# Performance work log

Hardware: AMD Instinct MI355X
Metric: run time of the kernel (lower is better)

## Reference

```python
import jax, jax.numpy as jnp
import numpy as np

B, S, E = 2, 2048, 1024
H = 16
D = E // H  # head_dim = 64


def setup_inputs() -> dict:
    key = jax.random.key(0)
    ks = jax.random.split(key, 11)
    s = 1.0 / np.sqrt(E)
    return {
        "x": jax.random.normal(ks[0], (B, S, E), dtype=jnp.float32),
        "Wq": jax.random.uniform(ks[1], (E, E), jnp.float32, -s, s),
        "bq": jnp.zeros((E,), jnp.float32),
        "Wk": jax.random.uniform(ks[2], (E, E), jnp.float32, -s, s),
        "bk": jnp.zeros((E,), jnp.float32),
        "Wv": jax.random.uniform(ks[3], (E, E), jnp.float32, -s, s),
        "bv": jnp.zeros((E,), jnp.float32),
        "Wo": jax.random.uniform(ks[4], (E, E), jnp.float32, -s, s),
        "bo": jnp.zeros((E,), jnp.float32),
        "J_attn": jax.random.normal(ks[5], (H, D, D), jnp.float32) * 0.02,
        "lambda_attn": jnp.float32(0.5),
    }


def reference(x, Wq, bq, Wk, bk, Wv, bv, Wo, bo, J_attn, lambda_attn):
    b, s, _ = x.shape
    scale = jnp.sqrt(jnp.float32(D))

    def split_heads(y):  # [b,s,E] -> [b,H,s,D]
        return y.reshape(b, s, H, D).transpose(0, 2, 1, 3)

    Q = split_heads(x @ Wq.T + bq)
    K = split_heads(x @ Wk.T + bk)
    V = split_heads(x @ Wv.T + bv)

    attn_scores = jnp.einsum('bhid,bhjd->bhij', Q, K) / scale

    Qn = jnp.tanh(Q)
    Kn = jnp.tanh(K)
    # fold J into Qn first (small [H,D,D] contraction), then one big matmul
    QJ = jnp.einsum('bhid,hde->bhie', Qn, J_attn)
    delta = jnp.einsum('bhie,bhje->bhij', QJ, Kn)

    attn_scores = attn_scores + lambda_attn * delta
    attn_probs = jax.nn.softmax(attn_scores, axis=-1)

    out = jnp.einsum('bhij,bhjd->bhid', attn_probs, V)
    out = out.transpose(0, 2, 1, 3).reshape(b, s, E)
    return out @ Wo.T + bo
```

## Files before the change

kernel.cpp:

```cpp
#include <hip/hip_runtime.h>
#include <math.h>

#define NH 16

typedef __bf16 bf16x8 __attribute__((ext_vector_type(8)));
typedef float f32x4 __attribute__((ext_vector_type(4)));

__device__ __forceinline__ unsigned short f2bf(float f) {
  unsigned u = __float_as_uint(f);
  u += 0x7fffu + ((u >> 16) & 1u);
  return (unsigned short)(u >> 16);
}
__device__ __forceinline__ float bf2f(unsigned short h) {
  return __uint_as_float(((unsigned)h) << 16);
}
__device__ __forceinline__ float fexp2(float x) {
  return __builtin_amdgcn_exp2f(x);
}
__device__ __forceinline__ float fast_tanh16(float x) {
  return 1.f - 2.f * __builtin_amdgcn_rcpf(fexp2(16.f * x) + 1.f);
}
__device__ __forceinline__ void gl_lds16(const void* g, void* l) {
  __builtin_amdgcn_global_load_lds((const __attribute__((address_space(1))) void*)g,
                                   (__attribute__((address_space(3))) void*)l, 16, 0, 0);
}
union Frag8 { bf16x8 v; unsigned short u[8]; };
union FragU { bf16x8 v; unsigned u[4]; };
union FragQ { bf16x8 v; unsigned long long q[2]; };

__global__ __launch_bounds__(256) void prep_all(const float* __restrict__ x,
                                                const float* __restrict__ Wq,
                                                const float* __restrict__ Wk,
                                                const float* __restrict__ Wv,
                                                const float* __restrict__ Wo,
                                                const float* __restrict__ J,
                                                const float* __restrict__ lam_p,
                                                unsigned short* __restrict__ xh,
                                                unsigned short* __restrict__ wcat3,
                                                unsigned short* __restrict__ wocat,
                                                unsigned short* __restrict__ Jt)
{
  __shared__ float T[64][65];
  const int bid = blockIdx.x, tid = threadIdx.x;
  if (bid >= 8192) {
    const int h = bid - 8192;
    const float lam = lam_p[0] * 1.44269504f;
#pragma unroll
    for (int c = 0; c < 4; ++c) {
      int i = tid + c*256;
      int d = i >> 4, e4 = i & 15;
      float4 v = *(const float4*)&J[(size_t)h*4096 + d*64 + e4*4];
      T[d][e4*4+0] = v.x; T[d][e4*4+1] = v.y; T[d][e4*4+2] = v.z; T[d][e4*4+3] = v.w;
    }
    __syncthreads();
    const int e = tid >> 2, d0 = (tid & 3) * 16;
#pragma unroll
    for (int j4 = 0; j4 < 4; ++j4) {
      ushort4 o;
      o.x = f2bf(lam * T[d0+j4*4+0][e]);
      o.y = f2bf(lam * T[d0+j4*4+1][e]);
      o.z = f2bf(lam * T[d0+j4*4+2][e]);
      o.w = f2bf(lam * T[d0+j4*4+3][e]);
      *(ushort4*)&Jt[((size_t)h*64 + e)*64 + d0 + j4*4] = o;
    }
    return;
  }
  if (bid < 4096) {
    int i = bid * 256 + tid;
    float4 v = *(const float4*)&x[(size_t)i*4];
    ushort4 o;
    o.x = f2bf(v.x); o.y = f2bf(v.y); o.z = f2bf(v.z); o.w = f2bf(v.w);
    *(ushort4*)&xh[(size_t)i*4] = o;
  } else if (bid < 7168) {
    int i = (bid - 4096) * 256 + tid;
    int sel = i >> 18, loc = i & 262143;
    const float* src = (sel == 0) ? Wq : (sel == 1) ? Wk : Wv;
    float4 v = *(const float4*)&src[(size_t)loc*4];
    ushort4 o;
    o.x = f2bf(v.x); o.y = f2bf(v.y); o.z = f2bf(v.z); o.w = f2bf(v.w);
    *(ushort4*)&wcat3[(size_t)i*4] = o;
  } else {
    int i = (bid - 7168) * 256 + tid;
    int r = i >> 8, c = i & 255;
    float4 v = *(const float4*)&Wo[(size_t)r*1024 + c*4];
    ushort4 hi, lo;
    hi.x = f2bf(v.x); lo.x = f2bf(v.x - bf2f(hi.x));
    hi.y = f2bf(v.y); lo.y = f2bf(v.y - bf2f(hi.y));
    hi.z = f2bf(v.z); lo.z = f2bf(v.z - bf2f(hi.z));
    hi.w = f2bf(v.w); lo.w = f2bf(v.w - bf2f(hi.w));
    *(ushort4*)&wocat[(size_t)r*2048 + c*4]        = hi;
    *(ushort4*)&wocat[(size_t)r*2048 + 1024 + c*4] = lo;
  }
}

__global__ __launch_bounds__(256) void gemm_qkv(const unsigned short* __restrict__ A,
                                                const unsigned short* __restrict__ W,
                                                const float* __restrict__ bq,
                                                const float* __restrict__ bk,
                                                const float* __restrict__ bv,
                                                const unsigned short* __restrict__ Jt,
                                                unsigned short* __restrict__ Qcat,
                                                unsigned short* __restrict__ Kcat,
                                                unsigned short* __restrict__ Vt)
{
  __shared__ unsigned short S[32768];
  const int tid = threadIdx.x, lane = tid & 63, wq = tid >> 6;
  const int l15 = lane & 15, lq = lane >> 4;
  const int n0 = blockIdx.x * 128, m0 = blockIdx.y * 128;
  const int wr = (wq & 1) * 64, wc = (wq >> 1) * 64;
  const int mode = n0 >> 10;

  f32x4 acc[4][4];
#pragma unroll
  for (int mb = 0; mb < 4; ++mb)
#pragma unroll
    for (int nb = 0; nb < 4; ++nb) { f32x4 z = {0.f,0.f,0.f,0.f}; acc[mb][nb] = z; }

  const unsigned short* mat = (wq < 2) ? A : W;
  const int rbase = (wq < 2) ? m0 : n0;
  const int srow = lane >> 3, sslot = lane & 7;

  auto STAGE = [&](int buf, int k0) {
    unsigned short* lb = S + buf*16384 + (wq >> 1) * 8192;
#pragma unroll
    for (int t = 0; t < 8; ++t) {
      int row = (wq & 1) * 64 + t*8 + srow;
      int chunk = sslot ^ (row & 7);
      gl_lds16(mat + (size_t)(rbase + row)*1024 + k0 + chunk*8,
               lb + ((wq & 1) * 64 + t*8) * 64);
    }
  };

  int cur = 0;
  STAGE(0, 0);
  __syncthreads();

  for (int k0 = 0; k0 < 1024; k0 += 64) {
    if (k0 + 64 < 1024) STAGE(cur ^ 1, k0 + 64);
    const unsigned short* Sc = S + cur*16384;
#pragma unroll
    for (int kk = 0; kk < 2; ++kk) {
      int c = kk*4 + lq;
      bf16x8 af[4], bf_[4];
#pragma unroll
      for (int mb = 0; mb < 4; ++mb) {
        int m = wr + mb*16 + l15;
        af[mb] = *(const bf16x8*)&Sc[m*64 + (c ^ (m & 7))*8];
      }
#pragma unroll
      for (int nb = 0; nb < 4; ++nb) {
        int n = wc + nb*16 + l15;
        bf_[nb] = *(const bf16x8*)&Sc[8192 + n*64 + (c ^ (n & 7))*8];
      }
#pragma unroll
      for (int mb = 0; mb < 4; ++mb)
#pragma unroll
        for (int nb = 0; nb < 4; ++nb)
          acc[mb][nb] = __builtin_amdgcn_mfma_f32_16x16x32_bf16(af[mb], bf_[nb], acc[mb][nb], 0,0,0);
    }
    __syncthreads();
    cur ^= 1;
  }

  const float* bias = (mode == 0) ? bq : (mode == 1) ? bk : bv;
  float bvv[4];
#pragma unroll
  for (int nb = 0; nb < 4; ++nb) bvv[nb] = bias[((n0 & 1023) + wc + nb*16 + l15)];

  if (mode == 2) {
#pragma unroll
    for (int mb = 0; mb < 4; ++mb) {
      int mrow = m0 + wr + mb*16 + lq*4;
      int b = mrow >> 11, s0 = mrow & 2047;
#pragma unroll
      for (int nb = 0; nb < 4; ++nb) {
        int n = (n0 & 1023) + wc + nb*16 + l15;
        int h = n >> 6, d = n & 63;
        ushort4 o;
        o.x = f2bf(acc[mb][nb][0] + bvv[nb]);
        o.y = f2bf(acc[mb][nb][1] + bvv[nb]);
        o.z = f2bf(acc[mb][nb][2] + bvv[nb]);
        o.w = f2bf(acc[mb][nb][3] + bvv[nb]);
        *(ushort4*)&Vt[((size_t)(b*NH + h)*64 + d)*2048 + s0] = o;
      }
    }
    return;
  }

  if (mode == 1) {
#pragma unroll
    for (int mb = 0; mb < 4; ++mb) {
#pragma unroll
      for (int r = 0; r < 4; ++r) {
        int m = m0 + wr + mb*16 + lq*4 + r;
        int b = m >> 11, s = m & 2047;
#pragma unroll
        for (int nb = 0; nb < 4; ++nb) {
          float v = acc[mb][nb][r] + bvv[nb];
          int n = (n0 & 1023) + wc + nb*16 + l15;
          int h = n >> 6, d = n & 63;
          size_t row = ((size_t)(b*NH + h)*2048 + s)*128;
          Kcat[row + d]      = f2bf(v);
          Kcat[row + 64 + d] = f2bf(1.f - 2.f * __builtin_amdgcn_rcpf(__expf(2.f*v) + 1.f));
        }
      }
    }
    return;
  }

  unsigned short* T = S + wq * 4608;
#pragma unroll
  for (int mb = 0; mb < 4; ++mb) {
#pragma unroll
    for (int r = 0; r < 4; ++r) {
      int m = m0 + wr + mb*16 + lq*4 + r;
      int b = m >> 11, s = m & 2047;
#pragma unroll
      for (int nb = 0; nb < 4; ++nb) {
        float v = acc[mb][nb][r] + bvv[nb];
        int n = (n0 & 1023) + wc + nb*16 + l15;
        int h = n >> 6, d = n & 63;
        unsigned short qb = f2bf(v * 0.18033688f);
        Qcat[((size_t)(b*NH + h)*2048 + s)*128 + d] = qb;
        T[(mb*16 + lq*4 + r)*72 + d] = qb;
      }
    }
  }
  const int h = ((n0 & 1023) + wc) >> 6;
  bf16x8 jf2[4][2];
#pragma unroll
  for (int nb2 = 0; nb2 < 4; ++nb2)
#pragma unroll
    for (int kst = 0; kst < 2; ++kst)
      jf2[nb2][kst] = *(const bf16x8*)&Jt[((size_t)h*64 + nb2*16 + l15)*64 + kst*32 + lq*8];
#pragma unroll
  for (int mb = 0; mb < 4; ++mb) {
    Frag8 af2[2];
#pragma unroll
    for (int kst = 0; kst < 2; ++kst) {
      Frag8 raw;
      raw.v = *(const bf16x8*)&T[(mb*16 + l15)*72 + kst*32 + lq*8];
#pragma unroll
      for (int j = 0; j < 8; ++j) {
        float t = fast_tanh16(bf2f(raw.u[j]));
        af2[kst].u[j] = (unsigned short)(__float_as_uint(t) >> 16);
      }
    }
    f32x4 a2[4];
#pragma unroll
    for (int nb2 = 0; nb2 < 4; ++nb2) { f32x4 z = {0.f,0.f,0.f,0.f}; a2[nb2] = z; }
#pragma unroll
    for (int kst = 0; kst < 2; ++kst)
#pragma unroll
      for (int nb2 = 0; nb2 < 4; ++nb2)
        a2[nb2] = __builtin_amdgcn_mfma_f32_16x16x32_bf16(af2[kst].v, jf2[nb2][kst], a2[nb2], 0,0,0);
    int mrow = m0 + wr + mb*16 + lq*4;
    int b = mrow >> 11, s0 = mrow & 2047;
#pragma unroll
    for (int r = 0; r < 4; ++r) {
      size_t rowb = ((size_t)(b*NH + h)*2048 + s0 + r)*128 + 64;
#pragma unroll
      for (int nb2 = 0; nb2 < 4; ++nb2)
        Qcat[rowb + nb2*16 + l15] = f2bf(a2[nb2][r]);
    }
  }
}

__global__ __launch_bounds__(256, 4) void flash8(
    const unsigned short* __restrict__ Qcat, const unsigned short* __restrict__ Kcat,
    const unsigned short* __restrict__ Vt, unsigned short* __restrict__ attcat)
{
  __shared__ __align__(16) char smem[49152];
  unsigned short* Ks = (unsigned short*)smem;
  unsigned short* Vs = (unsigned short*)(smem + 32768);
  const int tid = threadIdx.x, lane = tid & 63, wq = tid >> 6;
  const int l15 = lane & 15, lq = lane >> 4;
  const int bid = blockIdx.x;
  const int bh = (((bid >> 3) & 3) << 3) | (bid & 7);
  const int inner = bid >> 5;
  const int row0 = inner * 128;

  Frag8 qf[2][4];
#pragma unroll
  for (int nb = 0; nb < 2; ++nb) {
    const unsigned short* qp = Qcat + ((size_t)(bh*2048 + row0 + wq*32 + nb*16 + l15))*128 + lq*8;
#pragma unroll
    for (int kst = 0; kst < 4; ++kst)
      qf[nb][kst].v = *(const bf16x8*)(qp + kst*32);
  }

  FragU ones;
  ones.u[0] = 0x3F803F80u; ones.u[1] = 0x3F803F80u;
  ones.u[2] = 0x3F803F80u; ones.u[3] = 0x3F803F80u;

  f32x4 o[4][2];
  f32x4 lacc[2];
  { f32x4 z = {0.f,0.f,0.f,0.f}; lacc[0] = z; lacc[1] = z; }
#pragma unroll
  for (int db = 0; db < 4; ++db)
#pragma unroll
    for (int nb = 0; nb < 2; ++nb) { f32x4 z = {0.f,0.f,0.f,0.f}; o[db][nb] = z; }

  const unsigned short* kgb = Kcat + ((size_t)bh*2048)*128;
  const unsigned short* vg  = Vt + (size_t)bh*64*2048;

  auto STAGE = [&](int buf, int jt) {
#pragma unroll
    for (int t = 0; t < 4; ++t) {
      int g = (wq*4 + t)*4 + (lane >> 4);
      int slot = lane & 15;
      int chunk = (slot & 8) | ((slot ^ g) & 7);
      gl_lds16(kgb + (size_t)(jt*64 + g)*128 + chunk*8, Ks + buf*8192 + (wq*4 + t)*512);
    }
#pragma unroll
    for (int t = 0; t < 2; ++t) {
      int rv = (wq*2 + t)*8 + (lane >> 3);
      int chunk = (lane & 7) ^ (rv & 7);
      gl_lds16(vg + (size_t)rv*2048 + jt*64 + chunk*8, Vs + buf*4096 + (wq*2 + t)*512);
    }
  };

  int cur = 0;
  STAGE(0, 0);
  __syncthreads();

  for (int jt = 0; jt < 32; ++jt) {
    if (jt + 1 < 32) STAGE(cur ^ 1, jt + 1);
    const unsigned short* ksb = Ks + cur*8192;
    const unsigned short* vsb = Vs + cur*4096;

#pragma unroll
    for (int t = 0; t < 2; ++t) {
      unsigned P2[2][2][2];
#pragma unroll
      for (int kk = 0; kk < 2; ++kk) {
        const int kb = 2*t + kk;
        bf16x8 af[4];
#pragma unroll
        for (int kst = 0; kst < 4; ++kst) {
          int key = kb*16 + l15;
          int c = kst*4 + lq;
          int slot = (c & 8) | ((c ^ key) & 7);
          af[kst] = *(const bf16x8*)&ksb[key*128 + slot*8];
        }
        f32x4 s[2];
        { f32x4 z = {0.f,0.f,0.f,0.f}; s[0] = z; s[1] = z; }
        __builtin_amdgcn_s_setprio(1);
#pragma unroll
        for (int kst = 0; kst < 4; ++kst) {
          s[0] = __builtin_amdgcn_mfma_f32_16x16x32_bf16(af[kst], qf[0][kst].v, s[0], 0,0,0);
          s[1] = __builtin_amdgcn_mfma_f32_16x16x32_bf16(af[kst], qf[1][kst].v, s[1], 0,0,0);
        }
        __builtin_amdgcn_s_setprio(0);
#pragma unroll
        for (int nb = 0; nb < 2; ++nb) {
          float e0 = fexp2(s[nb][0]), e1 = fexp2(s[nb][1]);
          float e2 = fexp2(s[nb][2]), e3 = fexp2(s[nb][3]);
          P2[nb][kk][0] = __builtin_amdgcn_perm(__float_as_uint(e1), __float_as_uint(e0), 0x07060302u);
          P2[nb][kk][1] = __builtin_amdgcn_perm(__float_as_uint(e3), __float_as_uint(e2), 0x07060302u);
        }
      }

      FragU bfr[2];
#pragma unroll
      for (int nb = 0; nb < 2; ++nb) {
        bfr[nb].u[0] = P2[nb][0][0];
        bfr[nb].u[1] = P2[nb][0][1];
        bfr[nb].u[2] = P2[nb][1][0];
        bfr[nb].u[3] = P2[nb][1][1];
      }
      __builtin_amdgcn_s_setprio(1);
      lacc[0] = __builtin_amdgcn_mfma_f32_16x16x32_bf16(ones.v, bfr[0].v, lacc[0], 0,0,0);
      lacc[1] = __builtin_amdgcn_mfma_f32_16x16x32_bf16(ones.v, bfr[1].v, lacc[1], 0,0,0);

      const int c0 = 4*t + (lq >> 1);
      const int woff = 4*(lq & 1);
#pragma unroll
      for (int db = 0; db < 4; ++db) {
        int d = db*16 + l15;
        FragQ va;
        va.q[0] = *(const unsigned long long*)&vsb[d*64 + ((c0     ^ (d & 7))*8) + woff];
        va.q[1] = *(const unsigned long long*)&vsb[d*64 + (((c0+2) ^ (d & 7))*8) + woff];
        o[db][0] = __builtin_amdgcn_mfma_f32_16x16x32_bf16(va.v, bfr[0].v, o[db][0], 0,0,0);
        o[db][1] = __builtin_amdgcn_mfma_f32_16x16x32_bf16(va.v, bfr[1].v, o[db][1], 0,0,0);
      }
      __builtin_amdgcn_s_setprio(0);
    }

    __syncthreads();
    cur ^= 1;
  }

  const int b = bh >> 4, h = bh & (NH-1);
  const float inv0 = 1.f / lacc[0][0];
  const float inv1 = 1.f / lacc[1][0];
  float* Ts = (float*)smem;
#pragma unroll
  for (int half = 0; half < 2; ++half) {
    __syncthreads();
    if ((wq >> 1) == half) {
#pragma unroll
      for (int nb = 0; nb < 2; ++nb) {
        const float inv = nb ? inv1 : inv0;
        const int rl = (wq & 1)*32 + nb*16 + l15;
#pragma unroll
        for (int db = 0; db < 4; ++db)
#pragma unroll
          for (int r = 0; r < 4; ++r)
            Ts[rl*65 + db*16 + lq*4 + r] = o[db][nb][r] * inv;
      }
    }
    __syncthreads();
    const int sl = tid >> 2, d0 = (tid & 3) * 16;
    const int srow = row0 + half*64 + sl;
    const size_t rb = ((size_t)(b*2048 + srow))*2048 + h*64;
#pragma unroll
    for (int j4 = 0; j4 < 4; ++j4) {
      float v0 = Ts[sl*65 + d0 + j4*4 + 0];
      float v1 = Ts[sl*65 + d0 + j4*4 + 1];
      float v2 = Ts[sl*65 + d0 + j4*4 + 2];
      float v3 = Ts[sl*65 + d0 + j4*4 + 3];
      ushort4 hi, lo;
      hi.x = f2bf(v0); lo.x = f2bf(v0 - bf2f(hi.x));
      hi.y = f2bf(v1); lo.y = f2bf(v1 - bf2f(hi.y));
      hi.z = f2bf(v2); lo.z = f2bf(v2 - bf2f(hi.z));
      hi.w = f2bf(v3); lo.w = f2bf(v3 - bf2f(hi.w));
      *(ushort4*)&attcat[rb + d0 + j4*4]        = hi;
      *(ushort4*)&attcat[rb + 1024 + d0 + j4*4] = lo;
    }
  }
}

__global__ __launch_bounds__(512) void gemm3b(const unsigned short* __restrict__ A,
                                              const unsigned short* __restrict__ W,
                                              const float* __restrict__ bias,
                                              float* __restrict__ out)
{
  __shared__ unsigned short S[65536];
  const int tid = threadIdx.x, lane = tid & 63, wid = tid >> 6;
  const int l15 = lane & 15, lq = lane >> 4;
  const int n0 = blockIdx.x * 128, m0 = blockIdx.y * 128;
  const int wrow = wid >> 2, wcol = wid & 3;

  f32x4 acc[4][2];
#pragma unroll
  for (int mb = 0; mb < 4; ++mb)
#pragma unroll
    for (int nb = 0; nb < 2; ++nb) { f32x4 z = {0.f,0.f,0.f,0.f}; acc[mb][nb] = z; }

  const int region = wid >> 1;
  const unsigned short* mat = (region < 2) ? A : W;
  const int rbase = (region < 2) ? m0 : n0;
  const int koff  = (region & 1) * 1024;
  const int rhalf = (wid & 1) * 64;
  const int srow = lane >> 3, sslot = lane & 7;

  auto STAGE = [&](int buf, int k0) {
    unsigned short* lb = S + buf*32768 + region*8192 + rhalf*64;
#pragma unroll
    for (int t = 0; t < 8; ++t) {
      int row = rhalf + t*8 + srow;
      int chunk = sslot ^ (row & 7);
      gl_lds16(mat + (size_t)(rbase + row)*2048 + koff + k0 + chunk*8,
               lb + t*512);
    }
  };

  int cur = 0;
  STAGE(0, 0);
  __syncthreads();

  for (int k0 = 0; k0 < 1024; k0 += 64) {
    if (k0 + 64 < 1024) STAGE(cur ^ 1, k0 + 64);
    const unsigned short* Sc = S + cur*32768;
#pragma unroll
    for (int kk = 0; kk < 2; ++kk) {
      int c = kk*4 + lq;
      bf16x8 ah[4], al[4], bh_[2], bl_[2];
#pragma unroll
      for (int mb = 0; mb < 4; ++mb) {
        int m = wrow*64 + mb*16 + l15;
        int so = (c ^ (m & 7))*8;
        ah[mb] = *(const bf16x8*)&Sc[m*64 + so];
        al[mb] = *(const bf16x8*)&Sc[8192 + m*64 + so];
      }
#pragma unroll
      for (int nb = 0; nb < 2; ++nb) {
        int n = wcol*32 + nb*16 + l15;
        int so = (c ^ (n & 7))*8;
        bh_[nb] = *(const bf16x8*)&Sc[16384 + n*64 + so];
        bl_[nb] = *(const bf16x8*)&Sc[24576 + n*64 + so];
      }
#pragma unroll
      for (int mb = 0; mb < 4; ++mb)
#pragma unroll
        for (int nb = 0; nb < 2; ++nb) {
          acc[mb][nb] = __builtin_amdgcn_mfma_f32_16x16x32_bf16(ah[mb], bh_[nb], acc[mb][nb], 0,0,0);
          acc[mb][nb] = __builtin_amdgcn_mfma_f32_16x16x32_bf16(al[mb], bh_[nb], acc[mb][nb], 0,0,0);
          acc[mb][nb] = __builtin_amdgcn_mfma_f32_16x16x32_bf16(ah[mb], bl_[nb], acc[mb][nb], 0,0,0);
        }
    }
    __syncthreads();
    cur ^= 1;
  }

  float bvv[2];
#pragma unroll
  for (int nb = 0; nb < 2; ++nb) bvv[nb] = bias[n0 + wcol*32 + nb*16 + l15];
#pragma unroll
  for (int mb = 0; mb < 4; ++mb)
#pragma unroll
    for (int r = 0; r < 4; ++r) {
      int m = m0 + wrow*64 + mb*16 + lq*4 + r;
#pragma unroll
      for (int nb = 0; nb < 2; ++nb) {
        int n = n0 + wcol*32 + nb*16 + l15;
        out[(size_t)m*1024 + n] = acc[mb][nb][r] + bvv[nb];
      }
    }
}

extern "C" void kernel_launch(void* const* d_in, const int* in_sizes, int n_in,
                              void* d_out, int out_size, void* d_ws, size_t ws_size,
                              hipStream_t stream)
{
  const float* x   = (const float*)d_in[0];
  const float* Wq  = (const float*)d_in[1];
  const float* bq  = (const float*)d_in[2];
  const float* Wk  = (const float*)d_in[3];
  const float* bk  = (const float*)d_in[4];
  const float* Wv  = (const float*)d_in[5];
  const float* bv  = (const float*)d_in[6];
  const float* Wo  = (const float*)d_in[7];
  const float* bo  = (const float*)d_in[8];
  const float* J   = (const float*)d_in[9];
  const float* lam = (const float*)d_in[10];

  char* p = (char*)d_ws;
  unsigned short* xh     = (unsigned short*)p;  p += (size_t)4096*1024*2;
  unsigned short* wcat3  = (unsigned short*)p;  p += (size_t)3072*1024*2;
  unsigned short* Jt     = (unsigned short*)p;  p += (size_t)16*64*64*2;
  p += (size_t)2*1024*1024;
  unsigned short* Qcat   = (unsigned short*)p;  p += (size_t)65536*128*2;
  unsigned short* Kcat   = (unsigned short*)p;  p += (size_t)65536*128*2;
  unsigned short* Vt     = (unsigned short*)p;  p += (size_t)32*64*2048*2;
  unsigned short* wocat  = (unsigned short*)p;  p += (size_t)1024*2048*2;
  unsigned short* attcat = (unsigned short*)p;  p += (size_t)4096*2048*2;
  float* out = (float*)d_out;

  dim3 blk(256);

  prep_all<<<dim3(8208), blk, 0, stream>>>(x, Wq, Wk, Wv, Wo, J, lam, xh, wcat3, wocat, Jt);
  gemm_qkv<<<dim3(24, 32), blk, 0, stream>>>(xh, wcat3, bq, bk, bv, Jt, Qcat, Kcat, Vt);
  flash8<<<dim3(512), blk, 0, stream>>>(Qcat, Kcat, Vt, attcat);
  gemm3b<<<dim3(8, 32), dim3(512), 0, stream>>>(attcat, wocat, bo, out);
}
```

Before: 221.5 us.

## Use 8 waves per flash block, each owning 16 query rows

The attention kernel moves from 4 waves of 32 query rows each to 8 waves of 16 rows each, with the block size doubled to 512 threads. Per-wave accumulators and Q fragments are halved, the K/V staging work is spread over more waves, and the epilogue is simplified to a single pass. This is meant to raise wave-level parallelism and latency hiding, but each wave now reads the K and V fragments from LDS for only half as many query rows, so LDS traffic per MFMA doubles.

```diff
diff --git a/kernel.cpp b/kernel.cpp
--- a/kernel.cpp
+++ b/kernel.cpp
@@ -266,7 +266,7 @@
   }
 }
 
-__global__ __launch_bounds__(256, 4) void flash8(
+__global__ __launch_bounds__(512, 4) void flash8(
     const unsigned short* __restrict__ Qcat, const unsigned short* __restrict__ Kcat,
     const unsigned short* __restrict__ Vt, unsigned short* __restrict__ attcat)
 {
@@ -280,43 +280,40 @@
   const int inner = bid >> 5;
   const int row0 = inner * 128;
 
-  Frag8 qf[2][4];
-#pragma unroll
-  for (int nb = 0; nb < 2; ++nb) {
-    const unsigned short* qp = Qcat + ((size_t)(bh*2048 + row0 + wq*32 + nb*16 + l15))*128 + lq*8;
+  Frag8 qf[4];
+  {
+    const unsigned short* qp = Qcat + ((size_t)(bh*2048 + row0 + wq*16 + l15))*128 + lq*8;
 #pragma unroll
     for (int kst = 0; kst < 4; ++kst)
-      qf[nb][kst].v = *(const bf16x8*)(qp + kst*32);
+      qf[kst].v = *(const bf16x8*)(qp + kst*32);
   }
 
   FragU ones;
   ones.u[0] = 0x3F803F80u; ones.u[1] = 0x3F803F80u;
   ones.u[2] = 0x3F803F80u; ones.u[3] = 0x3F803F80u;
 
-  f32x4 o[4][2];
-  f32x4 lacc[2];
-  { f32x4 z = {0.f,0.f,0.f,0.f}; lacc[0] = z; lacc[1] = z; }
-#pragma unroll
-  for (int db = 0; db < 4; ++db)
-#pragma unroll
-    for (int nb = 0; nb < 2; ++nb) { f32x4 z = {0.f,0.f,0.f,0.f}; o[db][nb] = z; }
+  f32x4 o[4];
+  f32x4 lacc;
+  { f32x4 z = {0.f,0.f,0.f,0.f}; lacc = z;
+#pragma unroll
+    for (int db = 0; db < 4; ++db) o[db] = z; }
 
   const unsigned short* kgb = Kcat + ((size_t)bh*2048)*128;
   const unsigned short* vg  = Vt + (size_t)bh*64*2048;
 
   auto STAGE = [&](int buf, int jt) {
 #pragma unroll
-    for (int t = 0; t < 4; ++t) {
-      int g = (wq*4 + t)*4 + (lane >> 4);
+    for (int t = 0; t < 2; ++t) {
+      int G = wq*2 + t;
+      int g = G*4 + (lane >> 4);
       int slot = lane & 15;
       int chunk = (slot & 8) | ((slot ^ g) & 7);
-      gl_lds16(kgb + (size_t)(jt*64 + g)*128 + chunk*8, Ks + buf*8192 + (wq*4 + t)*512);
-    }
-#pragma unroll
-    for (int t = 0; t < 2; ++t) {
-      int rv = (wq*2 + t)*8 + (lane >> 3);
+      gl_lds16(kgb + (size_t)(jt*64 + g)*128 + chunk*8, Ks + buf*8192 + G*512);
+    }
+    {
+      int rv = wq*8 + (lane >> 3);
       int chunk = (lane & 7) ^ (rv & 7);
-      gl_lds16(vg + (size_t)rv*2048 + jt*64 + chunk*8, Vs + buf*4096 + (wq*2 + t)*512);
+      gl_lds16(vg + (size_t)rv*2048 + jt*64 + chunk*8, Vs + buf*4096 + wq*512);
     }
   };
 
@@ -331,7 +328,7 @@
 
 #pragma unroll
     for (int t = 0; t < 2; ++t) {
-      unsigned P2[2][2][2];
+      unsigned P2[2][2];
 #pragma unroll
       for (int kk = 0; kk < 2; ++kk) {
         const int kb = 2*t + kk;
@@ -343,35 +340,26 @@
           int slot = (c & 8) | ((c ^ key) & 7);
           af[kst] = *(const bf16x8*)&ksb[key*128 + slot*8];
         }
-        f32x4 s[2];
-        { f32x4 z = {0.f,0.f,0.f,0.f}; s[0] = z; s[1] = z; }
+        f32x4 s;
+        { f32x4 z = {0.f,0.f,0.f,0.f}; s = z; }
         __builtin_amdgcn_s_setprio(1);
 #pragma unroll
-        for (int kst = 0; kst < 4; ++kst) {
-          s[0] = __builtin_amdgcn_mfma_f32_16x16x32_bf16(af[kst], qf[0][kst].v, s[0], 0,0,0);
-          s[1] = __builtin_amdgcn_mfma_f32_16x16x32_bf16(af[kst], qf[1][kst].v, s[1], 0,0,0);
-        }
+        for (int kst = 0; kst < 4; ++kst)
+          s = __builtin_amdgcn_mfma_f32_16x16x32_bf16(af[kst], qf[kst].v, s, 0,0,0);
         __builtin_amdgcn_s_setprio(0);
-#pragma unroll
-        for (int nb = 0; nb < 2; ++nb) {
-          float e0 = fexp2(s[nb][0]), e1 = fexp2(s[nb][1]);
-          float e2 = fexp2(s[nb][2]), e3 = fexp2(s[nb][3]);
-          P2[nb][kk][0] = __builtin_amdgcn_perm(__float_as_uint(e1), __float_as_uint(e0), 0x07060302u);
-          P2[nb][kk][1] = __builtin_amdgcn_perm(__float_as_uint(e3), __float_as_uint(e2), 0x07060302u);
-        }
-      }
-
-      FragU bfr[2];
-#pragma unroll
-      for (int nb = 0; nb < 2; ++nb) {
-        bfr[nb].u[0] = P2[nb][0][0];
-        bfr[nb].u[1] = P2[nb][0][1];
-        bfr[nb].u[2] = P2[nb][1][0];
-        bfr[nb].u[3] = P2[nb][1][1];
-      }
+        float e0 = fexp2(s[0]), e1 = fexp2(s[1]);
+        float e2 = fexp2(s[2]), e3 = fexp2(s[3]);
+        P2[kk][0] = __builtin_amdgcn_perm(__float_as_uint(e1), __float_as_uint(e0), 0x07060302u);
+        P2[kk][1] = __builtin_amdgcn_perm(__float_as_uint(e3), __float_as_uint(e2), 0x07060302u);
+      }
+
+      FragU bfr;
+      bfr.u[0] = P2[0][0];
+      bfr.u[1] = P2[0][1];
+      bfr.u[2] = P2[1][0];
+      bfr.u[3] = P2[1][1];
       __builtin_amdgcn_s_setprio(1);
-      lacc[0] = __builtin_amdgcn_mfma_f32_16x16x32_bf16(ones.v, bfr[0].v, lacc[0], 0,0,0);
-      lacc[1] = __builtin_amdgcn_mfma_f32_16x16x32_bf16(ones.v, bfr[1].v, lacc[1], 0,0,0);
+      lacc = __builtin_amdgcn_mfma_f32_16x16x32_bf16(ones.v, bfr.v, lacc, 0,0,0);
 
       const int c0 = 4*t + (lq >> 1);
       const int woff = 4*(lq & 1);
@@ -381,8 +369,7 @@
         FragQ va;
         va.q[0] = *(const unsigned long long*)&vsb[d*64 + ((c0     ^ (d & 7))*8) + woff];
         va.q[1] = *(const unsigned long long*)&vsb[d*64 + (((c0+2) ^ (d & 7))*8) + woff];
-        o[db][0] = __builtin_amdgcn_mfma_f32_16x16x32_bf16(va.v, bfr[0].v, o[db][0], 0,0,0);
-        o[db][1] = __builtin_amdgcn_mfma_f32_16x16x32_bf16(va.v, bfr[1].v, o[db][1], 0,0,0);
+        o[db] = __builtin_amdgcn_mfma_f32_16x16x32_bf16(va.v, bfr.v, o[db], 0,0,0);
       }
       __builtin_amdgcn_s_setprio(0);
     }
@@ -392,42 +379,30 @@
   }
 
   const int b = bh >> 4, h = bh & (NH-1);
-  const float inv0 = 1.f / lacc[0][0];
-  const float inv1 = 1.f / lacc[1][0];
+  const float inv = 1.f / lacc[0];
   float* Ts = (float*)smem;
-#pragma unroll
-  for (int half = 0; half < 2; ++half) {
-    __syncthreads();
-    if ((wq >> 1) == half) {
-#pragma unroll
-      for (int nb = 0; nb < 2; ++nb) {
-        const float inv = nb ? inv1 : inv0;
-        const int rl = (wq & 1)*32 + nb*16 + l15;
-#pragma unroll
-        for (int db = 0; db < 4; ++db)
-#pragma unroll
-          for (int r = 0; r < 4; ++r)
-            Ts[rl*65 + db*16 + lq*4 + r] = o[db][nb][r] * inv;
-      }
-    }
-    __syncthreads();
-    const int sl = tid >> 2, d0 = (tid & 3) * 16;
-    const int srow = row0 + half*64 + sl;
-    const size_t rb = ((size_t)(b*2048 + srow))*2048 + h*64;
-#pragma unroll
-    for (int j4 = 0; j4 < 4; ++j4) {
-      float v0 = Ts[sl*65 + d0 + j4*4 + 0];
-      float v1 = Ts[sl*65 + d0 + j4*4 + 1];
-      float v2 = Ts[sl*65 + d0 + j4*4 + 2];
-      float v3 = Ts[sl*65 + d0 + j4*4 + 3];
-      ushort4 hi, lo;
-      hi.x = f2bf(v0); lo.x = f2bf(v0 - bf2f(hi.x));
-      hi.y = f2bf(v1); lo.y = f2bf(v1 - bf2f(hi.y));
-      hi.z = f2bf(v2); lo.z = f2bf(v2 - bf2f(hi.z));
-      hi.w = f2bf(v3); lo.w = f2bf(v3 - bf2f(hi.w));
-      *(ushort4*)&attcat[rb + d0 + j4*4]        = hi;
-      *(ushort4*)&attcat[rb + 1024 + d0 + j4*4] = lo;
-    }
+  __syncthreads();
+#pragma unroll
+  for (int db = 0; db < 4; ++db)
+#pragma unroll
+    for (int r = 0; r < 4; ++r)
+      Ts[(wq*16 + l15)*65 + db*16 + lq*4 + r] = o[db][r] * inv;
+  __syncthreads();
+  const int sl = tid >> 2, d0 = (tid & 3) * 16;
+  const size_t rb = ((size_t)(b*2048 + row0 + sl))*2048 + h*64;
+#pragma unroll
+  for (int j4 = 0; j4 < 4; ++j4) {
+    float v0 = Ts[sl*65 + d0 + j4*4 + 0];
+    float v1 = Ts[sl*65 + d0 + j4*4 + 1];
+    float v2 = Ts[sl*65 + d0 + j4*4 + 2];
+    float v3 = Ts[sl*65 + d0 + j4*4 + 3];
+    ushort4 hi, lo;
+    hi.x = f2bf(v0); lo.x = f2bf(v0 - bf2f(hi.x));
+    hi.y = f2bf(v1); lo.y = f2bf(v1 - bf2f(hi.y));
+    hi.z = f2bf(v2); lo.z = f2bf(v2 - bf2f(hi.z));
+    hi.w = f2bf(v3); lo.w = f2bf(v3 - bf2f(hi.w));
+    *(ushort4*)&attcat[rb + d0 + j4*4]        = hi;
+    *(ushort4*)&attcat[rb + 1024 + d0 + j4*4] = lo;
   }
 }
 
@@ -552,6 +527,6 @@
 
   prep_all<<<dim3(8208), blk, 0, stream>>>(x, Wq, Wk, Wv, Wo, J, lam, xh, wcat3, wocat, Jt);
   gemm_qkv<<<dim3(24, 32), blk, 0, stream>>>(xh, wcat3, bq, bk, bv, Jt, Qcat, Kcat, Vt);
-  flash8<<<dim3(512), blk, 0, stream>>>(Qcat, Kcat, Vt, attcat);
+  flash8<<<dim3(512), dim3(512), 0, stream>>>(Qcat, Kcat, Vt, attcat);
   gemm3b<<<dim3(8, 32), dim3(512), 0, stream>>>(attcat, wocat, bo, out);
 }
```

Measured after the change: 223.2 us. Within noise of the previous version (+0.8%).
